# Kernel tuning notes

Measured on AMD Instinct MI355X. Metric: run time of the kernel, lower is better.

Reference implementation:

```python
import jax, jax.numpy as jnp
import numpy as np

L, H = 4, 8
BIAS_STEP = 25
LN_EPS = 1e-5

def make_pe(T, D):
    pos = np.arange(T)[:, None].astype(np.float32)
    div = np.exp(np.arange(0, D, 2).astype(np.float32) * (-np.log(10000.0) / D))
    pe = np.zeros((T, D), np.float32)
    pe[:, 0::2] = np.sin(pos * div)
    pe[:, 1::2] = np.cos(pos * div)
    return jnp.asarray(pe)

def make_band_mask(T):
    # (H, T, T) bool, True = masked out. Head h attends within |i-j| <= BIAS_STEP*(h+1).
    i = np.arange(T)
    dist = np.abs(i[:, None] - i[None, :])
    win = (np.arange(H) + 1) * BIAS_STEP
    return jnp.asarray(dist[None, :, :] > win[:, None, None])

def layer_norm(x, g, b):
    m = x.mean(-1, keepdims=True)
    v = ((x - m) ** 2).mean(-1, keepdims=True)
    return (x - m) * jax.lax.rsqrt(v + LN_EPS) * g + b

def setup_inputs() -> dict:
    key = jax.random.key(0)
    ks = jax.random.split(key, 16)
    s = 0.02
    BS, T, IN, D, FF, C = 8, 1000, 256, 512, 2048, 8
    return {
        'x': jax.random.normal(ks[0], (BS, T, IN), jnp.float32),
        'Wemb': jax.random.normal(ks[1], (D, IN), jnp.float32) * s,
        'bemb': jnp.zeros((D,), jnp.float32),
        'Wqkv': jax.random.normal(ks[2], (L, 3 * D, D), jnp.float32) * s,
        'bqkv': jnp.zeros((L, 3 * D), jnp.float32),
        'Wo': jax.random.normal(ks[3], (L, D, D), jnp.float32) * s,
        'bo': jnp.zeros((L, D), jnp.float32),
        'W1': jax.random.normal(ks[4], (L, FF, D), jnp.float32) * s,
        'b1f': jnp.zeros((L, FF), jnp.float32),
        'W2': jax.random.normal(ks[5], (L, D, FF), jnp.float32) * s,
        'b2f': jnp.zeros((L, D), jnp.float32),
        'g1': jnp.ones((L, D), jnp.float32),
        'be1': jnp.zeros((L, D), jnp.float32),
        'g2': jnp.ones((L, D), jnp.float32),
        'be2': jnp.zeros((L, D), jnp.float32),
        'Wcls': jax.random.normal(ks[6], (C, D), jnp.float32) * s,
        'bcls': jnp.zeros((C,), jnp.float32),
    }

def reference(x, Wemb, bemb, Wqkv, bqkv, Wo, bo, W1, b1f, W2, b2f, g1, be1, g2, be2, Wcls, bcls):
    bs, T, _ = x.shape
    D = Wemb.shape[0]
    dh = D // H
    h = x @ Wemb.T + bemb                     # (bs,T,D) input embedding
    h = h + make_pe(T, D)[None]               # sinusoidal PE (dropout=0)
    mask = make_band_mask(T)                  # (H,T,T)
    neg = jnp.finfo(h.dtype).min
    for l in range(L):                        # post-norm TransformerEncoderLayer
        qkv = h @ Wqkv[l].T + bqkv[l]
        q, k, v = jnp.split(qkv, 3, axis=-1)
        q = q.reshape(bs, T, H, dh).transpose(0, 2, 1, 3)
        k = k.reshape(bs, T, H, dh).transpose(0, 2, 1, 3)
        v = v.reshape(bs, T, H, dh).transpose(0, 2, 1, 3)
        s = jnp.einsum('bhqd,bhkd->bhqk', q, k) / jnp.sqrt(jnp.asarray(dh, h.dtype))
        s = jnp.where(mask[None], neg, s)
        a = jax.nn.softmax(s, axis=-1)
        o = jnp.einsum('bhqk,bhkd->bhqd', a, v).transpose(0, 2, 1, 3).reshape(bs, T, D)
        o = o @ Wo[l].T + bo[l]
        h = layer_norm(h + o, g1[l], be1[l])
        ff = jax.nn.relu(h @ W1[l].T + b1f[l]) @ W2[l].T + b2f[l]
        h = layer_norm(h + ff, g2[l], be2[l])
    pooled = h.max(axis=1)                    # global max pool over time (max_pool=True)
    logits = pooled @ Wcls.T + bcls
    return jax.nn.log_softmax(logits, axis=1)
```

## Files before the change

### kernel.cpp

```cpp
#include <hip/hip_runtime.h>
#include <math.h>

#define T_SEQ   1000
#define BATCH   8
#define DMODEL  512
#define NHEAD   8
#define DHEAD   64
#define FFDIM   2048
#define NLAYER  4
#define MROWS   (BATCH * T_SEQ)
#define TCHUNK  25

typedef __bf16 bf16x8 __attribute__((ext_vector_type(8)));
typedef __bf16 bf16x4 __attribute__((ext_vector_type(4)));
typedef float  f32x4  __attribute__((ext_vector_type(4)));
typedef float  f32x16 __attribute__((ext_vector_type(16)));

#define GL2LDS(g, l) \
    __builtin_amdgcn_global_load_lds((const __attribute__((address_space(1))) void*)(g), \
                                     (__attribute__((address_space(3))) void*)(l), 16, 0, 0)

__global__ __launch_bounds__(256)
void f2bf(const float* __restrict__ in, __bf16* __restrict__ out)
{
    int i = (blockIdx.x * 256 + threadIdx.x) * 4;
    float4 v = *(const float4*)(in + i);
    bf16x4 o;
    o[0] = (__bf16)v.x; o[1] = (__bf16)v.y; o[2] = (__bf16)v.z; o[3] = (__bf16)v.w;
    *(bf16x4*)(out + i) = o;
}

template<bool WF32, bool WBF16, bool RELU, bool PE>
__global__ __launch_bounds__(256)
void gemm_bf16(const __bf16* __restrict__ A, const __bf16* __restrict__ B,
               const float* __restrict__ bias, float* __restrict__ Cf,
               __bf16* __restrict__ Cb, int M, int N, int K)
{
    __shared__ __align__(16) __bf16 As[3][64 * 64];
    __shared__ __align__(16) __bf16 Bs[3][128 * 64];

    const int tid  = threadIdx.x;
    const int lane = tid & 63;
    const int w    = tid >> 6;
    const int wr   = w >> 1, wc = w & 1;
    const int row0 = blockIdx.y * 64;
    const int col0 = blockIdx.x * 128;

    size_t aoffg[2], boffg[4];
    int    ldso[4];
    #pragma unroll
    for (int p = 0; p < 4; ++p) {
        const int bo = p * 4096 + tid * 16;
        const int r  = bo >> 7;
        const int cs = (bo & 127) ^ ((r & 7) << 4);
        if (p < 2) aoffg[p] = (size_t)(row0 + r) * K * 2 + cs;
        boffg[p] = (size_t)(col0 + r) * K * 2 + cs;
        ldso[p]  = bo;
    }

    f32x4 acc[2][4];
    #pragma unroll
    for (int m = 0; m < 2; ++m)
        #pragma unroll
        for (int n = 0; n < 4; ++n) acc[m][n] = (f32x4)0.f;

    const char* gA = (const char*)A;
    const char* gB = (const char*)B;
    const int nt = K >> 6;

    auto STAGE = [&](int tt, int buf) {
        const size_t kb = (size_t)tt << 7;
        char* lA = (char*)As[buf];
        char* lB = (char*)Bs[buf];
        #pragma unroll
        for (int p = 0; p < 2; ++p) GL2LDS(gA + aoffg[p] + kb, lA + ldso[p]);
        #pragma unroll
        for (int p = 0; p < 4; ++p) GL2LDS(gB + boffg[p] + kb, lB + ldso[p]);
    };

    STAGE(0, 0);
    STAGE(1, 1);
    asm volatile("s_waitcnt vmcnt(6)" ::: "memory");
    __builtin_amdgcn_s_barrier();
    __builtin_amdgcn_sched_barrier(0);

    int bc = 0, bn = 2;
    for (int t = 0; t < nt; ++t) {
        if (t + 2 < nt) STAGE(t + 2, bn);
        const char* as = (const char*)As[bc];
        const char* bs = (const char*)Bs[bc];
        __builtin_amdgcn_s_setprio(1);
        #pragma unroll
        for (int ks = 0; ks < 2; ++ks) {
            bf16x8 af[2], bfr[4];
            const int cb = ks * 64 + (lane >> 4) * 16;
            #pragma unroll
            for (int m = 0; m < 2; ++m) {
                const int rr = wr * 32 + m * 16 + (lane & 15);
                af[m] = *(const bf16x8*)(as + rr * 128 + (cb ^ ((rr & 7) << 4)));
            }
            #pragma unroll
            for (int n = 0; n < 4; ++n) {
                const int rr = wc * 64 + n * 16 + (lane & 15);
                bfr[n] = *(const bf16x8*)(bs + rr * 128 + (cb ^ ((rr & 7) << 4)));
            }
            #pragma unroll
            for (int m = 0; m < 2; ++m)
                #pragma unroll
                for (int n = 0; n < 4; ++n)
                    acc[m][n] = __builtin_amdgcn_mfma_f32_16x16x32_bf16(af[m], bfr[n], acc[m][n], 0, 0, 0);
        }
        __builtin_amdgcn_s_setprio(0);
        if (t + 2 < nt) { asm volatile("s_waitcnt vmcnt(6)" ::: "memory"); }
        else            { asm volatile("s_waitcnt vmcnt(0)" ::: "memory"); }
        __builtin_amdgcn_s_barrier();
        __builtin_amdgcn_sched_barrier(0);
        bc = bc + 1; if (bc == 3) bc = 0;
        bn = bn + 1; if (bn == 3) bn = 0;
    }

    const int crow = (lane >> 4) * 4;
    const int ccol = lane & 15;
    #pragma unroll
    for (int n = 0; n < 4; ++n) {
        const int gc = col0 + wc * 64 + n * 16 + ccol;
        const float bv = bias[gc];
        float freq = 0.f;
        if (PE) freq = __expf((float)(gc & ~1) * (-9.210340371976184f / (float)DMODEL));
        #pragma unroll
        for (int m = 0; m < 2; ++m) {
            const int gr0 = row0 + wr * 32 + m * 16 + crow;
            #pragma unroll
            for (int r = 0; r < 4; ++r) {
                const int gr = gr0 + r;
                float v = acc[m][n][r] + bv;
                if (PE) {
                    const int tt = gr % T_SEQ;
                    const float ang = (float)tt * freq;
                    v += (gc & 1) ? __cosf(ang) : __sinf(ang);
                }
                if (RELU) v = fmaxf(v, 0.f);
                if (WF32)  Cf[(size_t)gr * N + gc] = v;
                if (WBF16) Cb[(size_t)gr * N + gc] = (__bf16)v;
            }
        }
    }
}

__global__ __launch_bounds__(256)
void attn_mfma(const __bf16* __restrict__ qkv, __bf16* __restrict__ o)
{
    const int wv   = (blockIdx.x << 2) + (threadIdx.x >> 6);
    const int lane = threadIdx.x & 63;
    const int qt   = wv & 31;
    const int hh   = (wv >> 5) & 7;
    const int b    = wv >> 8;
    const int qb   = qt * 32;
    const int half = lane >> 5;
    const int ql   = lane & 31;
    const int i    = qb + ql;
    const int iq   = (i < T_SEQ) ? i : (T_SEQ - 1);

    const int RS = 3 * DMODEL;
    const __bf16* Q = qkv + (size_t)b * T_SEQ * RS + hh * DHEAD;
    const __bf16* K = Q + DMODEL;
    const __bf16* V = Q + 2 * DMODEL;

    bf16x8 qf[4];
    {
        const __bf16* qrow = Q + (size_t)iq * RS + half * 8;
        #pragma unroll
        for (int ds = 0; ds < 4; ++ds)
            qf[ds] = *(const bf16x8*)(qrow + ds * 16);
    }

    const int w = 25 * (hh + 1);
    const int kb_lo = (qb - w > 0 ? qb - w : 0) & ~31;
    const int kb_hi = (qb + 31 + w < T_SEQ - 1) ? (qb + 31 + w) : (T_SEQ - 1);
    const int  spanv = (2 * w < T_SEQ - 1 - i + w) ? 2 * w : (T_SEQ - 1 - i + w);
    const unsigned span = (unsigned)spanv;
    const float C2 = 0.125f * 1.44269504089f;

    float m2 = -1e9f, l = 0.f;
    f32x16 oa0 = (f32x16)0.f, oa1 = (f32x16)0.f;

    for (int kb = kb_lo; kb <= kb_hi; kb += 32) {
        f32x16 sv = (f32x16)0.f;
        {
            int krow = kb + ql; if (krow > T_SEQ - 1) krow = T_SEQ - 1;
            const __bf16* kr = K + (size_t)krow * RS + half * 8;
            #pragma unroll
            for (int ds = 0; ds < 4; ++ds) {
                bf16x8 kf = *(const bf16x8*)(kr + ds * 16);
                sv = __builtin_amdgcn_mfma_f32_32x32x16_bf16(kf, qf[ds], sv, 0, 0, 0);
            }
        }

        const int base = kb - i + w;
        float s2[16];
        #pragma unroll
        for (int r = 0; r < 16; ++r) {
            const int kr = (r & 3) + 8 * (r >> 2) + 4 * half;
            const unsigned jrel = (unsigned)(base + kr);
            s2[r] = (jrel <= span) ? sv[r] * C2 : -1e9f;
        }

        float mx = s2[0];
        #pragma unroll
        for (int r = 1; r < 16; ++r) mx = fmaxf(mx, s2[r]);
        mx = fmaxf(mx, __shfl_xor(mx, 32, 64));

        if (!__all(mx <= m2 + 8.0f)) {
            const float mnew  = fmaxf(m2, mx);
            const float scale = exp2f(m2 - mnew);
            m2 = mnew;
            l *= scale;
            #pragma unroll
            for (int r = 0; r < 16; ++r) {
                const int qsrc = (r & 3) + 8 * (r >> 2) + 4 * half;
                const float sc = __shfl(scale, qsrc, 64);
                oa0[r] *= sc;
                oa1[r] *= sc;
            }
        }

        float p[16];
        float ps = 0.f;
        #pragma unroll
        for (int r = 0; r < 16; ++r) { p[r] = exp2f(s2[r] - m2); ps += p[r]; }
        ps += __shfl_xor(ps, 32, 64);
        l += ps;

        unsigned pk[8];
        #pragma unroll
        for (int t = 0; t < 8; ++t) {
            union { unsigned u; __bf16 h[2]; } cv;
            cv.h[0] = (__bf16)p[2 * t];
            cv.h[1] = (__bf16)p[2 * t + 1];
            pk[t] = cv.u;
        }
        unsigned y[8];
        #pragma unroll
        for (int t = 0; t < 8; ++t)
            y[t] = (unsigned)__shfl_xor((int)pk[t], 32, 64);

        union { unsigned u[4]; bf16x8 v; } pa0, pa1;
        if (half == 0) {
            pa0.u[0] = pk[0]; pa0.u[1] = pk[1]; pa0.u[2] = y[0];  pa0.u[3] = y[1];
            pa1.u[0] = pk[4]; pa1.u[1] = pk[5]; pa1.u[2] = y[4];  pa1.u[3] = y[5];
        } else {
            pa0.u[0] = y[2];  pa0.u[1] = y[3];  pa0.u[2] = pk[2]; pa0.u[3] = pk[3];
            pa1.u[0] = y[6];  pa1.u[1] = y[7];  pa1.u[2] = pk[6]; pa1.u[3] = pk[7];
        }

        #pragma unroll
        for (int ks = 0; ks < 2; ++ks) {
            const int R0 = kb + ks * 16 + half * 8;
            #pragma unroll
            for (int dh = 0; dh < 2; ++dh) {
                bf16x8 vf;
                const __bf16* vcol = V + dh * 32 + ql;
                #pragma unroll
                for (int j = 0; j < 8; ++j) {
                    int rr = R0 + j; if (rr > T_SEQ - 1) rr = T_SEQ - 1;
                    vf[j] = vcol[(size_t)rr * RS];
                }
                if (dh == 0)
                    oa0 = __builtin_amdgcn_mfma_f32_32x32x16_bf16(ks ? pa1.v : pa0.v, vf, oa0, 0, 0, 0);
                else
                    oa1 = __builtin_amdgcn_mfma_f32_32x32x16_bf16(ks ? pa1.v : pa0.v, vf, oa1, 0, 0, 0);
            }
        }
    }

    const float rinv = 1.f / l;
    __bf16* ob = o + ((size_t)b * T_SEQ) * DMODEL + hh * DHEAD;
    #pragma unroll
    for (int r = 0; r < 16; ++r) {
        const int q   = (r & 3) + 8 * (r >> 2) + 4 * half;
        const int row = qb + q;
        const float ri = __shfl(rinv, q, 64);
        if (row < T_SEQ) {
            ob[(size_t)row * DMODEL + ql]      = (__bf16)(oa0[r] * ri);
            ob[(size_t)row * DMODEL + 32 + ql] = (__bf16)(oa1[r] * ri);
        }
    }
}

__global__ __launch_bounds__(256)
void add_ln(float* __restrict__ hbuf, const __bf16* __restrict__ tbuf,
            const float* __restrict__ g, const float* __restrict__ b,
            __bf16* __restrict__ hb)
{
    const int row  = blockIdx.x * 4 + (threadIdx.x >> 6);
    const int lane = threadIdx.x & 63;
    float*        hp = hbuf + (size_t)row * DMODEL + lane * 8;
    const __bf16* tp = tbuf + (size_t)row * DMODEL + lane * 8;

    float xv[8];
    float4 h0 = *(const float4*)hp;   float4 h1 = *(const float4*)(hp + 4);
    bf16x8 tv = *(const bf16x8*)tp;
    xv[0] = h0.x + (float)tv[0]; xv[1] = h0.y + (float)tv[1];
    xv[2] = h0.z + (float)tv[2]; xv[3] = h0.w + (float)tv[3];
    xv[4] = h1.x + (float)tv[4]; xv[5] = h1.y + (float)tv[5];
    xv[6] = h1.z + (float)tv[6]; xv[7] = h1.w + (float)tv[7];

    float s = 0.f;
    #pragma unroll
    for (int j = 0; j < 8; ++j) s += xv[j];
    #pragma unroll
    for (int off = 32; off >= 1; off >>= 1) s += __shfl_xor(s, off, 64);
    float mean = s * (1.f / DMODEL);

    float vs = 0.f;
    #pragma unroll
    for (int j = 0; j < 8; ++j) { float d = xv[j] - mean; vs += d * d; }
    #pragma unroll
    for (int off = 32; off >= 1; off >>= 1) vs += __shfl_xor(vs, off, 64);
    float rstd = rsqrtf(vs * (1.f / DMODEL) + 1e-5f);

    float4 g0 = *(const float4*)(g + lane * 8);
    float4 g1 = *(const float4*)(g + lane * 8 + 4);
    float4 b0 = *(const float4*)(b + lane * 8);
    float4 b1 = *(const float4*)(b + lane * 8 + 4);
    float gg[8] = {g0.x, g0.y, g0.z, g0.w, g1.x, g1.y, g1.z, g1.w};
    float bb[8] = {b0.x, b0.y, b0.z, b0.w, b1.x, b1.y, b1.z, b1.w};

    float outv[8];
    bf16x8 ob;
    #pragma unroll
    for (int j = 0; j < 8; ++j) {
        outv[j] = (xv[j] - mean) * rstd * gg[j] + bb[j];
        ob[j] = (__bf16)outv[j];
    }
    *(float4*)hp       = *(float4*)&outv[0];
    *(float4*)(hp + 4) = *(float4*)&outv[4];
    *(bf16x8*)(hb + (size_t)row * DMODEL + lane * 8) = ob;
}

__global__ __launch_bounds__(256)
void pool_p1(const float* __restrict__ hbuf, float* __restrict__ part)
{
    const int bb  = blockIdx.x;
    const int tc  = blockIdx.y;
    const int tid = threadIdx.x;
    const int t0  = tc * (T_SEQ / TCHUNK);
    const float* p = hbuf + ((size_t)bb * T_SEQ + t0) * DMODEL;

    float mx0 = -3.4e38f, mx1 = -3.4e38f;
    for (int t = 0; t < T_SEQ / TCHUNK; ++t) {
        mx0 = fmaxf(mx0, p[(size_t)t * DMODEL + tid]);
        mx1 = fmaxf(mx1, p[(size_t)t * DMODEL + 256 + tid]);
    }
    float* q = part + ((size_t)bb * TCHUNK + tc) * DMODEL;
    q[tid]       = mx0;
    q[tid + 256] = mx1;
}

__global__ __launch_bounds__(256)
void pool_p2(const float* __restrict__ part, const float* __restrict__ Wcls,
             const float* __restrict__ bcls, float* __restrict__ out)
{
    __shared__ float pooled[DMODEL];
    __shared__ float logits[8];
    const int bb  = blockIdx.x;
    const int tid = threadIdx.x;

    const float* q = part + (size_t)bb * TCHUNK * DMODEL;
    #pragma unroll
    for (int u = 0; u < 2; ++u) {
        const int d = tid + u * 256;
        float mx = -3.4e38f;
        for (int c = 0; c < TCHUNK; ++c) mx = fmaxf(mx, q[(size_t)c * DMODEL + d]);
        pooled[d] = mx;
    }
    __syncthreads();

    const int cls  = tid >> 5;
    const int lsub = tid & 31;
    const float* wr = Wcls + cls * DMODEL;
    float s = 0.f;
    #pragma unroll
    for (int u = 0; u < 16; ++u) {
        const int d = lsub + u * 32;
        s = fmaf(pooled[d], wr[d], s);
    }
    #pragma unroll
    for (int off = 16; off >= 1; off >>= 1) s += __shfl_xor(s, off, 32);
    if (lsub == 0) logits[cls] = s + bcls[cls];
    __syncthreads();

    if (tid == 0) {
        float mx = logits[0];
        for (int c = 1; c < 8; ++c) mx = fmaxf(mx, logits[c]);
        float se = 0.f;
        for (int c = 0; c < 8; ++c) se += expf(logits[c] - mx);
        float lse = logf(se) + mx;
        for (int c = 0; c < 8; ++c) out[bb * 8 + c] = logits[c] - lse;
    }
}

extern "C" void kernel_launch(void* const* d_in, const int* in_sizes, int n_in,
                              void* d_out, int out_size, void* d_ws, size_t ws_size,
                              hipStream_t stream)
{
    const float* x    = (const float*)d_in[0];
    const float* Wemb = (const float*)d_in[1];
    const float* bemb = (const float*)d_in[2];
    const float* Wqkv = (const float*)d_in[3];
    const float* bqkv = (const float*)d_in[4];
    const float* Wo   = (const float*)d_in[5];
    const float* bo   = (const float*)d_in[6];
    const float* W1   = (const float*)d_in[7];
    const float* b1f  = (const float*)d_in[8];
    const float* W2   = (const float*)d_in[9];
    const float* b2f  = (const float*)d_in[10];
    const float* g1   = (const float*)d_in[11];
    const float* be1  = (const float*)d_in[12];
    const float* g2   = (const float*)d_in[13];
    const float* be2  = (const float*)d_in[14];
    const float* Wcls = (const float*)d_in[15];
    const float* bcls = (const float*)d_in[16];
    float* out = (float*)d_out;

    float*  h    = (float*)d_ws;
    float*  tmpF = h + (size_t)MROWS * DMODEL;
    __bf16* hb   = (__bf16*)(tmpF + (size_t)MROWS * DMODEL);
    __bf16* qkvb = hb + (size_t)MROWS * DMODEL;
    __bf16* attb = qkvb + (size_t)MROWS * 3 * DMODEL;
    __bf16* ff1b = qkvb;
    __bf16* xb   = attb + (size_t)MROWS * DMODEL;
    __bf16* tmpB = xb + (size_t)MROWS * 256;
    __bf16* wb   = tmpB + (size_t)MROWS * DMODEL;
    __bf16* wEmb = wb;
    __bf16* wQKV = wEmb + 512 * 256;
    __bf16* wWo  = wQKV + (size_t)NLAYER * 3 * DMODEL * DMODEL;
    __bf16* wW1  = wWo  + (size_t)NLAYER * DMODEL * DMODEL;
    __bf16* wW2  = wW1  + (size_t)NLAYER * FFDIM * DMODEL;

    dim3 blk(256);

    f2bf<<<dim3(MROWS * 256 / 1024), blk, 0, stream>>>(x, xb);
    f2bf<<<dim3(512 * 256 / 1024), blk, 0, stream>>>(Wemb, wEmb);
    f2bf<<<dim3(NLAYER * 3 * DMODEL * DMODEL / 1024), blk, 0, stream>>>(Wqkv, wQKV);
    f2bf<<<dim3(NLAYER * DMODEL * DMODEL / 1024), blk, 0, stream>>>(Wo, wWo);
    f2bf<<<dim3(NLAYER * FFDIM * DMODEL / 1024), blk, 0, stream>>>(W1, wW1);
    f2bf<<<dim3(NLAYER * DMODEL * FFDIM / 1024), blk, 0, stream>>>(W2, wW2);

    gemm_bf16<true, true, false, true><<<dim3(4, 125), blk, 0, stream>>>(
        xb, wEmb, bemb, h, hb, MROWS, DMODEL, 256);

    for (int l = 0; l < NLAYER; ++l) {
        gemm_bf16<false, true, false, false><<<dim3(12, 125), blk, 0, stream>>>(
            hb, wQKV + (size_t)l * 3 * DMODEL * DMODEL, bqkv + (size_t)l * 3 * DMODEL,
            nullptr, qkvb, MROWS, 3 * DMODEL, DMODEL);
        attn_mfma<<<dim3(512), blk, 0, stream>>>(qkvb, attb);
        gemm_bf16<false, true, false, false><<<dim3(4, 125), blk, 0, stream>>>(
            attb, wWo + (size_t)l * DMODEL * DMODEL, bo + (size_t)l * DMODEL,
            nullptr, tmpB, MROWS, DMODEL, DMODEL);
        add_ln<<<dim3(MROWS / 4), blk, 0, stream>>>(
            h, tmpB, g1 + (size_t)l * DMODEL, be1 + (size_t)l * DMODEL, hb);
        gemm_bf16<false, true, true, false><<<dim3(16, 125), blk, 0, stream>>>(
            hb, wW1 + (size_t)l * FFDIM * DMODEL, b1f + (size_t)l * FFDIM,
            nullptr, ff1b, MROWS, FFDIM, DMODEL);
        gemm_bf16<false, true, false, false><<<dim3(4, 125), blk, 0, stream>>>(
            ff1b, wW2 + (size_t)l * DMODEL * FFDIM, b2f + (size_t)l * DMODEL,
            nullptr, tmpB, MROWS, DMODEL, FFDIM);
        add_ln<<<dim3(MROWS / 4), blk, 0, stream>>>(
            h, tmpB, g2 + (size_t)l * DMODEL, be2 + (size_t)l * DMODEL, hb);
    }

    pool_p1<<<dim3(BATCH, TCHUNK), blk, 0, stream>>>(h, tmpF);
    pool_p2<<<dim3(BATCH), blk, 0, stream>>>(tmpF, Wcls, bcls, out);
}
```

Measured before the change: 674.6 us.

## Write V transposed from QKV GEMM, pair heads per wave, keep residual in bf16

The QKV GEMM epilogue now splits its output: Q and K go to a compact 1024-wide buffer, and V is written transposed per batch and head so attention can read V fragments as contiguous 16-byte vectors instead of strided scalar gathers. The P·V MFMA operands are swapped so the output accumulator is per-query-row, and the rescale is a plain vector multiply rather than per-element shuffles. Each wave now processes two heads with complementary window sizes (ph and 7-ph) to balance work, and fully unmasked key blocks skip the band-mask compare. The fp32 residual stream is dropped; the residual is kept only in bf16, cutting LN and pooling traffic at some cost in accuracy, and the transposed V writes are scattered stores in the GEMM epilogue.

```diff
diff --git a/kernel.cpp b/kernel.cpp
--- a/kernel.cpp
+++ b/kernel.cpp
@@ -10,6 +10,8 @@
 #define NLAYER  4
 #define MROWS   (BATCH * T_SEQ)
 #define TCHUNK  25
+#define QKS     1024
+#define VTS     1024
 
 typedef __bf16 bf16x8 __attribute__((ext_vector_type(8)));
 typedef __bf16 bf16x4 __attribute__((ext_vector_type(4)));
@@ -30,11 +32,11 @@
     *(bf16x4*)(out + i) = o;
 }
 
-template<bool WF32, bool WBF16, bool RELU, bool PE>
+template<int MODE, bool RELU>
 __global__ __launch_bounds__(256)
 void gemm_bf16(const __bf16* __restrict__ A, const __bf16* __restrict__ B,
-               const float* __restrict__ bias, float* __restrict__ Cf,
-               __bf16* __restrict__ Cb, int M, int N, int K)
+               const float* __restrict__ bias, __bf16* __restrict__ Cb,
+               __bf16* __restrict__ Vt, int M, int N, int K)
 {
     __shared__ __align__(16) __bf16 As[3][64 * 64];
     __shared__ __align__(16) __bf16 Bs[3][128 * 64];
@@ -126,7 +128,7 @@
         const int gc = col0 + wc * 64 + n * 16 + ccol;
         const float bv = bias[gc];
         float freq = 0.f;
-        if (PE) freq = __expf((float)(gc & ~1) * (-9.210340371976184f / (float)DMODEL));
+        if (MODE == 1) freq = __expf((float)(gc & ~1) * (-9.210340371976184f / (float)DMODEL));
         #pragma unroll
         for (int m = 0; m < 2; ++m) {
             const int gr0 = row0 + wr * 32 + m * 16 + crow;
@@ -134,176 +136,187 @@
             for (int r = 0; r < 4; ++r) {
                 const int gr = gr0 + r;
                 float v = acc[m][n][r] + bv;
-                if (PE) {
+                if (MODE == 1) {
                     const int tt = gr % T_SEQ;
                     const float ang = (float)tt * freq;
                     v += (gc & 1) ? __cosf(ang) : __sinf(ang);
                 }
                 if (RELU) v = fmaxf(v, 0.f);
-                if (WF32)  Cf[(size_t)gr * N + gc] = v;
-                if (WBF16) Cb[(size_t)gr * N + gc] = (__bf16)v;
+                if (MODE == 2) {
+                    const int bidx = gr / T_SEQ;
+                    const int tt   = gr - bidx * T_SEQ;
+                    if (gc < 1024) {
+                        Cb[(size_t)gr * QKS + gc] = (__bf16)v;
+                    } else {
+                        Vt[((size_t)(bidx * DMODEL + (gc - 1024)) << 10) + tt] = (__bf16)v;
+                    }
+                } else {
+                    Cb[(size_t)gr * N + gc] = (__bf16)v;
+                }
             }
         }
     }
 }
 
 __global__ __launch_bounds__(256)
-void attn_mfma(const __bf16* __restrict__ qkv, __bf16* __restrict__ o)
+void attn_mfma(const __bf16* __restrict__ qkb, const __bf16* __restrict__ vt,
+               __bf16* __restrict__ o)
 {
     const int wv   = (blockIdx.x << 2) + (threadIdx.x >> 6);
     const int lane = threadIdx.x & 63;
-    const int qt   = wv & 31;
-    const int hh   = (wv >> 5) & 7;
-    const int b    = wv >> 8;
+    const int ph   = wv & 3;
+    const int qt   = (wv >> 2) & 31;
+    const int b    = wv >> 7;
     const int qb   = qt * 32;
     const int half = lane >> 5;
     const int ql   = lane & 31;
     const int i    = qb + ql;
     const int iq   = (i < T_SEQ) ? i : (T_SEQ - 1);
-
-    const int RS = 3 * DMODEL;
-    const __bf16* Q = qkv + (size_t)b * T_SEQ * RS + hh * DHEAD;
-    const __bf16* K = Q + DMODEL;
-    const __bf16* V = Q + 2 * DMODEL;
-
-    bf16x8 qf[4];
-    {
-        const __bf16* qrow = Q + (size_t)iq * RS + half * 8;
-        #pragma unroll
-        for (int ds = 0; ds < 4; ++ds)
-            qf[ds] = *(const bf16x8*)(qrow + ds * 16);
-    }
-
-    const int w = 25 * (hh + 1);
-    const int kb_lo = (qb - w > 0 ? qb - w : 0) & ~31;
-    const int kb_hi = (qb + 31 + w < T_SEQ - 1) ? (qb + 31 + w) : (T_SEQ - 1);
-    const int  spanv = (2 * w < T_SEQ - 1 - i + w) ? 2 * w : (T_SEQ - 1 - i + w);
-    const unsigned span = (unsigned)spanv;
     const float C2 = 0.125f * 1.44269504089f;
 
-    float m2 = -1e9f, l = 0.f;
-    f32x16 oa0 = (f32x16)0.f, oa1 = (f32x16)0.f;
-
-    for (int kb = kb_lo; kb <= kb_hi; kb += 32) {
-        f32x16 sv = (f32x16)0.f;
+    const __bf16* QKb = qkb + (size_t)b * T_SEQ * QKS;
+
+    #pragma unroll
+    for (int jb = 0; jb < 2; ++jb) {
+        const int hh = jb ? (7 - ph) : ph;
+        const __bf16* Q = QKb + hh * DHEAD;
+        const __bf16* K = Q + 512;
+        const __bf16* Vb = vt + (((size_t)b * DMODEL + hh * DHEAD) << 10);
+
+        bf16x8 qf[4];
         {
-            int krow = kb + ql; if (krow > T_SEQ - 1) krow = T_SEQ - 1;
-            const __bf16* kr = K + (size_t)krow * RS + half * 8;
-            #pragma unroll
-            for (int ds = 0; ds < 4; ++ds) {
-                bf16x8 kf = *(const bf16x8*)(kr + ds * 16);
-                sv = __builtin_amdgcn_mfma_f32_32x32x16_bf16(kf, qf[ds], sv, 0, 0, 0);
-            }
+            const __bf16* qrow = Q + (size_t)iq * QKS + half * 8;
+            #pragma unroll
+            for (int ds = 0; ds < 4; ++ds)
+                qf[ds] = *(const bf16x8*)(qrow + ds * 16);
         }
 
-        const int base = kb - i + w;
-        float s2[16];
-        #pragma unroll
-        for (int r = 0; r < 16; ++r) {
-            const int kr = (r & 3) + 8 * (r >> 2) + 4 * half;
-            const unsigned jrel = (unsigned)(base + kr);
-            s2[r] = (jrel <= span) ? sv[r] * C2 : -1e9f;
+        const int w = 25 * (hh + 1);
+        const int kb_lo = (qb - w > 0 ? qb - w : 0) & ~31;
+        const int kb_hi = (qb + 31 + w < T_SEQ - 1) ? (qb + 31 + w) : (T_SEQ - 1);
+        const int spanv = (2 * w < T_SEQ - 1 - i + w) ? 2 * w : (T_SEQ - 1 - i + w);
+        const unsigned span = (unsigned)spanv;
+
+        float m2 = -1e9f, l = 0.f;
+        f32x16 oa0 = (f32x16)0.f, oa1 = (f32x16)0.f;
+
+        for (int kb = kb_lo; kb <= kb_hi; kb += 32) {
+            f32x16 sv = (f32x16)0.f;
+            {
+                int krow = kb + ql; if (krow > T_SEQ - 1) krow = T_SEQ - 1;
+                const __bf16* kr = K + (size_t)krow * QKS + half * 8;
+                #pragma unroll
+                for (int ds = 0; ds < 4; ++ds) {
+                    bf16x8 kf = *(const bf16x8*)(kr + ds * 16);
+                    sv = __builtin_amdgcn_mfma_f32_32x32x16_bf16(kf, qf[ds], sv, 0, 0, 0);
+                }
+            }
+
+            const bool full = (kb >= qb + 31 - w) && (kb + 31 <= qb + w)
+                           && (kb + 31 <= T_SEQ - 1);
+            float s2[16];
+            if (full) {
+                #pragma unroll
+                for (int r = 0; r < 16; ++r) s2[r] = sv[r] * C2;
+            } else {
+                const int base = kb - i + w;
+                #pragma unroll
+                for (int r = 0; r < 16; ++r) {
+                    const int kr = (r & 3) + 8 * (r >> 2) + 4 * half;
+                    const unsigned jrel = (unsigned)(base + kr);
+                    s2[r] = (jrel <= span) ? sv[r] * C2 : -1e9f;
+                }
+            }
+
+            float mx = s2[0];
+            #pragma unroll
+            for (int r = 1; r < 16; ++r) mx = fmaxf(mx, s2[r]);
+            mx = fmaxf(mx, __shfl_xor(mx, 32, 64));
+
+            if (!__all(mx <= m2 + 8.0f)) {
+                const float mnew  = fmaxf(m2, mx);
+                const float scale = exp2f(m2 - mnew);
+                m2 = mnew;
+                l *= scale;
+                oa0 *= scale;
+                oa1 *= scale;
+            }
+
+            float p[16];
+            float ps = 0.f;
+            #pragma unroll
+            for (int r = 0; r < 16; ++r) { p[r] = exp2f(s2[r] - m2); ps += p[r]; }
+            ps += __shfl_xor(ps, 32, 64);
+            l += ps;
+
+            unsigned pk[8];
+            #pragma unroll
+            for (int t = 0; t < 8; ++t) {
+                union { unsigned u; __bf16 h[2]; } cv;
+                cv.h[0] = (__bf16)p[2 * t];
+                cv.h[1] = (__bf16)p[2 * t + 1];
+                pk[t] = cv.u;
+            }
+            unsigned y[8];
+            #pragma unroll
+            for (int t = 0; t < 8; ++t)
+                y[t] = (unsigned)__shfl_xor((int)pk[t], 32, 64);
+
+            union { unsigned u[4]; bf16x8 v; } pa0, pa1;
+            if (half == 0) {
+                pa0.u[0] = pk[0]; pa0.u[1] = pk[1]; pa0.u[2] = y[0];  pa0.u[3] = y[1];
+                pa1.u[0] = pk[4]; pa1.u[1] = pk[5]; pa1.u[2] = y[4];  pa1.u[3] = y[5];
+            } else {
+                pa0.u[0] = y[2];  pa0.u[1] = y[3];  pa0.u[2] = pk[2]; pa0.u[3] = pk[3];
+                pa1.u[0] = y[6];  pa1.u[1] = y[7];  pa1.u[2] = pk[6]; pa1.u[3] = pk[7];
+            }
+
+            #pragma unroll
+            for (int ks = 0; ks < 2; ++ks) {
+                const int kc = kb + ks * 16 + half * 8;
+                #pragma unroll
+                for (int dh = 0; dh < 2; ++dh) {
+                    const bf16x8 vf = *(const bf16x8*)(Vb + (((size_t)(dh * 32 + ql)) << 10) + kc);
+                    if (dh == 0)
+                        oa0 = __builtin_amdgcn_mfma_f32_32x32x16_bf16(vf, ks ? pa1.v : pa0.v, oa0, 0, 0, 0);
+                    else
+                        oa1 = __builtin_amdgcn_mfma_f32_32x32x16_bf16(vf, ks ? pa1.v : pa0.v, oa1, 0, 0, 0);
+                }
+            }
         }
 
-        float mx = s2[0];
-        #pragma unroll
-        for (int r = 1; r < 16; ++r) mx = fmaxf(mx, s2[r]);
-        mx = fmaxf(mx, __shfl_xor(mx, 32, 64));
-
-        if (!__all(mx <= m2 + 8.0f)) {
-            const float mnew  = fmaxf(m2, mx);
-            const float scale = exp2f(m2 - mnew);
-            m2 = mnew;
-            l *= scale;
-            #pragma unroll
-            for (int r = 0; r < 16; ++r) {
-                const int qsrc = (r & 3) + 8 * (r >> 2) + 4 * half;
-                const float sc = __shfl(scale, qsrc, 64);
-                oa0[r] *= sc;
-                oa1[r] *= sc;
+        if (i < T_SEQ) {
+            const float ri = 1.f / l;
+            __bf16* orow = o + (size_t)(b * T_SEQ + i) * DMODEL + hh * DHEAD;
+            #pragma unroll
+            for (int g = 0; g < 4; ++g) {
+                bf16x4 v0, v1;
+                #pragma unroll
+                for (int r = 0; r < 4; ++r) {
+                    v0[r] = (__bf16)(oa0[g * 4 + r] * ri);
+                    v1[r] = (__bf16)(oa1[g * 4 + r] * ri);
+                }
+                *(bf16x4*)(orow + g * 8 + half * 4)      = v0;
+                *(bf16x4*)(orow + 32 + g * 8 + half * 4) = v1;
             }
         }
-
-        float p[16];
-        float ps = 0.f;
-        #pragma unroll
-        for (int r = 0; r < 16; ++r) { p[r] = exp2f(s2[r] - m2); ps += p[r]; }
-        ps += __shfl_xor(ps, 32, 64);
-        l += ps;
-
-        unsigned pk[8];
-        #pragma unroll
-        for (int t = 0; t < 8; ++t) {
-            union { unsigned u; __bf16 h[2]; } cv;
-            cv.h[0] = (__bf16)p[2 * t];
-            cv.h[1] = (__bf16)p[2 * t + 1];
-            pk[t] = cv.u;
-        }
-        unsigned y[8];
-        #pragma unroll
-        for (int t = 0; t < 8; ++t)
-            y[t] = (unsigned)__shfl_xor((int)pk[t], 32, 64);
-
-        union { unsigned u[4]; bf16x8 v; } pa0, pa1;
-        if (half == 0) {
-            pa0.u[0] = pk[0]; pa0.u[1] = pk[1]; pa0.u[2] = y[0];  pa0.u[3] = y[1];
-            pa1.u[0] = pk[4]; pa1.u[1] = pk[5]; pa1.u[2] = y[4];  pa1.u[3] = y[5];
-        } else {
-            pa0.u[0] = y[2];  pa0.u[1] = y[3];  pa0.u[2] = pk[2]; pa0.u[3] = pk[3];
-            pa1.u[0] = y[6];  pa1.u[1] = y[7];  pa1.u[2] = pk[6]; pa1.u[3] = pk[7];
-        }
-
-        #pragma unroll
-        for (int ks = 0; ks < 2; ++ks) {
-            const int R0 = kb + ks * 16 + half * 8;
-            #pragma unroll
-            for (int dh = 0; dh < 2; ++dh) {
-                bf16x8 vf;
-                const __bf16* vcol = V + dh * 32 + ql;
-                #pragma unroll
-                for (int j = 0; j < 8; ++j) {
-                    int rr = R0 + j; if (rr > T_SEQ - 1) rr = T_SEQ - 1;
-                    vf[j] = vcol[(size_t)rr * RS];
-                }
-                if (dh == 0)
-                    oa0 = __builtin_amdgcn_mfma_f32_32x32x16_bf16(ks ? pa1.v : pa0.v, vf, oa0, 0, 0, 0);
-                else
-                    oa1 = __builtin_amdgcn_mfma_f32_32x32x16_bf16(ks ? pa1.v : pa0.v, vf, oa1, 0, 0, 0);
-            }
-        }
-    }
-
-    const float rinv = 1.f / l;
-    __bf16* ob = o + ((size_t)b * T_SEQ) * DMODEL + hh * DHEAD;
-    #pragma unroll
-    for (int r = 0; r < 16; ++r) {
-        const int q   = (r & 3) + 8 * (r >> 2) + 4 * half;
-        const int row = qb + q;
-        const float ri = __shfl(rinv, q, 64);
-        if (row < T_SEQ) {
-            ob[(size_t)row * DMODEL + ql]      = (__bf16)(oa0[r] * ri);
-            ob[(size_t)row * DMODEL + 32 + ql] = (__bf16)(oa1[r] * ri);
-        }
-    }
-}
-
-__global__ __launch_bounds__(256)
-void add_ln(float* __restrict__ hbuf, const __bf16* __restrict__ tbuf,
-            const float* __restrict__ g, const float* __restrict__ b,
-            __bf16* __restrict__ hb)
+    }
+}
+
+__global__ __launch_bounds__(256)
+void add_ln(__bf16* __restrict__ hb, const __bf16* __restrict__ tbuf,
+            const float* __restrict__ g, const float* __restrict__ b)
 {
     const int row  = blockIdx.x * 4 + (threadIdx.x >> 6);
     const int lane = threadIdx.x & 63;
-    float*        hp = hbuf + (size_t)row * DMODEL + lane * 8;
+    __bf16*       hp = hb   + (size_t)row * DMODEL + lane * 8;
     const __bf16* tp = tbuf + (size_t)row * DMODEL + lane * 8;
 
+    bf16x8 hv = *(const bf16x8*)hp;
+    bf16x8 tv = *(const bf16x8*)tp;
     float xv[8];
-    float4 h0 = *(const float4*)hp;   float4 h1 = *(const float4*)(hp + 4);
-    bf16x8 tv = *(const bf16x8*)tp;
-    xv[0] = h0.x + (float)tv[0]; xv[1] = h0.y + (float)tv[1];
-    xv[2] = h0.z + (float)tv[2]; xv[3] = h0.w + (float)tv[3];
-    xv[4] = h1.x + (float)tv[4]; xv[5] = h1.y + (float)tv[5];
-    xv[6] = h1.z + (float)tv[6]; xv[7] = h1.w + (float)tv[7];
+    #pragma unroll
+    for (int j = 0; j < 8; ++j) xv[j] = (float)hv[j] + (float)tv[j];
 
     float s = 0.f;
     #pragma unroll
@@ -326,31 +339,26 @@
     float gg[8] = {g0.x, g0.y, g0.z, g0.w, g1.x, g1.y, g1.z, g1.w};
     float bb[8] = {b0.x, b0.y, b0.z, b0.w, b1.x, b1.y, b1.z, b1.w};
 
-    float outv[8];
     bf16x8 ob;
     #pragma unroll
-    for (int j = 0; j < 8; ++j) {
-        outv[j] = (xv[j] - mean) * rstd * gg[j] + bb[j];
-        ob[j] = (__bf16)outv[j];
-    }
-    *(float4*)hp       = *(float4*)&outv[0];
-    *(float4*)(hp + 4) = *(float4*)&outv[4];
-    *(bf16x8*)(hb + (size_t)row * DMODEL + lane * 8) = ob;
-}
-
-__global__ __launch_bounds__(256)
-void pool_p1(const float* __restrict__ hbuf, float* __restrict__ part)
+    for (int j = 0; j < 8; ++j)
+        ob[j] = (__bf16)((xv[j] - mean) * rstd * gg[j] + bb[j]);
+    *(bf16x8*)hp = ob;
+}
+
+__global__ __launch_bounds__(256)
+void pool_p1(const __bf16* __restrict__ hb, float* __restrict__ part)
 {
     const int bb  = blockIdx.x;
     const int tc  = blockIdx.y;
     const int tid = threadIdx.x;
     const int t0  = tc * (T_SEQ / TCHUNK);
-    const float* p = hbuf + ((size_t)bb * T_SEQ + t0) * DMODEL;
+    const __bf16* p = hb + ((size_t)bb * T_SEQ + t0) * DMODEL;
 
     float mx0 = -3.4e38f, mx1 = -3.4e38f;
     for (int t = 0; t < T_SEQ / TCHUNK; ++t) {
-        mx0 = fmaxf(mx0, p[(size_t)t * DMODEL + tid]);
-        mx1 = fmaxf(mx1, p[(size_t)t * DMODEL + 256 + tid]);
+        mx0 = fmaxf(mx0, (float)p[(size_t)t * DMODEL + tid]);
+        mx1 = fmaxf(mx1, (float)p[(size_t)t * DMODEL + 256 + tid]);
     }
     float* q = part + ((size_t)bb * TCHUNK + tc) * DMODEL;
     q[tid]       = mx0;
@@ -423,20 +431,19 @@
     const float* bcls = (const float*)d_in[16];
     float* out = (float*)d_out;
 
-    float*  h    = (float*)d_ws;
-    float*  tmpF = h + (size_t)MROWS * DMODEL;
-    __bf16* hb   = (__bf16*)(tmpF + (size_t)MROWS * DMODEL);
-    __bf16* qkvb = hb + (size_t)MROWS * DMODEL;
-    __bf16* attb = qkvb + (size_t)MROWS * 3 * DMODEL;
-    __bf16* ff1b = qkvb;
-    __bf16* xb   = attb + (size_t)MROWS * DMODEL;
-    __bf16* tmpB = xb + (size_t)MROWS * 256;
-    __bf16* wb   = tmpB + (size_t)MROWS * DMODEL;
-    __bf16* wEmb = wb;
+    __bf16* hb   = (__bf16*)d_ws;
+    __bf16* qkb  = hb   + (size_t)MROWS * DMODEL;
+    __bf16* vtb  = qkb  + (size_t)MROWS * QKS;
+    __bf16* attb = vtb  + (size_t)BATCH * DMODEL * VTS;
+    __bf16* ff1b = attb + (size_t)MROWS * DMODEL;
+    __bf16* tmpB = ff1b + (size_t)MROWS * FFDIM;
+    __bf16* xb   = tmpB + (size_t)MROWS * DMODEL;
+    __bf16* wEmb = xb   + (size_t)MROWS * 256;
     __bf16* wQKV = wEmb + 512 * 256;
     __bf16* wWo  = wQKV + (size_t)NLAYER * 3 * DMODEL * DMODEL;
     __bf16* wW1  = wWo  + (size_t)NLAYER * DMODEL * DMODEL;
     __bf16* wW2  = wW1  + (size_t)NLAYER * FFDIM * DMODEL;
+    float*  partF = (float*)(wW2 + (size_t)NLAYER * DMODEL * FFDIM);
 
     dim3 blk(256);
 
@@ -447,29 +454,29 @@
     f2bf<<<dim3(NLAYER * FFDIM * DMODEL / 1024), blk, 0, stream>>>(W1, wW1);
     f2bf<<<dim3(NLAYER * DMODEL * FFDIM / 1024), blk, 0, stream>>>(W2, wW2);
 
-    gemm_bf16<true, true, false, true><<<dim3(4, 125), blk, 0, stream>>>(
-        xb, wEmb, bemb, h, hb, MROWS, DMODEL, 256);
+    gemm_bf16<1, false><<<dim3(4, 125), blk, 0, stream>>>(
+        xb, wEmb, bemb, hb, nullptr, MROWS, DMODEL, 256);
 
     for (int l = 0; l < NLAYER; ++l) {
-        gemm_bf16<false, true, false, false><<<dim3(12, 125), blk, 0, stream>>>(
+        gemm_bf16<2, false><<<dim3(12, 125), blk, 0, stream>>>(
             hb, wQKV + (size_t)l * 3 * DMODEL * DMODEL, bqkv + (size_t)l * 3 * DMODEL,
-            nullptr, qkvb, MROWS, 3 * DMODEL, DMODEL);
-        attn_mfma<<<dim3(512), blk, 0, stream>>>(qkvb, attb);
-        gemm_bf16<false, true, false, false><<<dim3(4, 125), blk, 0, stream>>>(
+            qkb, vtb, MROWS, 3 * DMODEL, DMODEL);
+        attn_mfma<<<dim3(256), blk, 0, stream>>>(qkb, vtb, attb);
+        gemm_bf16<0, false><<<dim3(4, 125), blk, 0, stream>>>(
             attb, wWo + (size_t)l * DMODEL * DMODEL, bo + (size_t)l * DMODEL,
-            nullptr, tmpB, MROWS, DMODEL, DMODEL);
+            tmpB, nullptr, MROWS, DMODEL, DMODEL);
         add_ln<<<dim3(MROWS / 4), blk, 0, stream>>>(
-            h, tmpB, g1 + (size_t)l * DMODEL, be1 + (size_t)l * DMODEL, hb);
-        gemm_bf16<false, true, true, false><<<dim3(16, 125), blk, 0, stream>>>(
+            hb, tmpB, g1 + (size_t)l * DMODEL, be1 + (size_t)l * DMODEL);
+        gemm_bf16<0, true><<<dim3(16, 125), blk, 0, stream>>>(
             hb, wW1 + (size_t)l * FFDIM * DMODEL, b1f + (size_t)l * FFDIM,
-            nullptr, ff1b, MROWS, FFDIM, DMODEL);
-        gemm_bf16<false, true, false, false><<<dim3(4, 125), blk, 0, stream>>>(
+            ff1b, nullptr, MROWS, FFDIM, DMODEL);
+        gemm_bf16<0, false><<<dim3(4, 125), blk, 0, stream>>>(
             ff1b, wW2 + (size_t)l * DMODEL * FFDIM, b2f + (size_t)l * DMODEL,
-            nullptr, tmpB, MROWS, DMODEL, FFDIM);
+            tmpB, nullptr, MROWS, DMODEL, FFDIM);
         add_ln<<<dim3(MROWS / 4), blk, 0, stream>>>(
-            h, tmpB, g2 + (size_t)l * DMODEL, be2 + (size_t)l * DMODEL, hb);
-    }
-
-    pool_p1<<<dim3(BATCH, TCHUNK), blk, 0, stream>>>(h, tmpF);
-    pool_p2<<<dim3(BATCH), blk, 0, stream>>>(tmpF, Wcls, bcls, out);
-}
+            hb, tmpB, g2 + (size_t)l * DMODEL, be2 + (size_t)l * DMODEL);
+    }
+
+    pool_p1<<<dim3(BATCH, TCHUNK), blk, 0, stream>>>(hb, partF);
+    pool_p2<<<dim3(BATCH), blk, 0, stream>>>(partF, Wcls, bcls, out);
+}
```

After: 693.2 us. +2.8%, slower.
